# Kernel tuning notes

Hardware: AMD Instinct MI355X
Metric: run time of the kernel (lower is better)

The kernel has to match this reference:

```python
import jax, jax.numpy as jnp
import numpy as np

# 8-bit signed quantizer bounds and integer-rescale constant (from module attrs)
X1_LO, X1_HI = -128.0, 127.0
X2_LO, X2_HI = -128.0, 127.0
Y_LO, Y_HI = -128.0, 127.0
G_VALUE = 16.0


def setup_inputs() -> dict:
    key = jax.random.key(0)
    k1, k2 = jax.random.split(key)
    # Pre-quantized integer activations stored as float32 (as in int-infer mode)
    x1 = jnp.round(jnp.clip(jax.random.normal(k1, (2, 16, 2048, 64), dtype=jnp.float32) * 40.0, X1_LO, X1_HI))
    x2 = jnp.round(jnp.clip(jax.random.normal(k2, (2, 16, 64, 2048), dtype=jnp.float32) * 40.0, X2_LO, X2_HI))
    return {
        "x1": x1,
        "x2": x2,
        "scale1_last_layer": jnp.float32(0.1),
        "scale_x1": jnp.float32(0.05),
        "scale2_last_layer": jnp.float32(0.08),
        "scale_x2": jnp.float32(0.04),
    }


def _div_shift(x, scale_prev, scale_cur, lo, hi):
    # round(x * s_prev / s_cur) then clamp to quantizer bounds
    return jnp.clip(jnp.round(x * (scale_prev / scale_cur)), lo, hi)


def reference(x1, x2, scale1_last_layer, scale_x1, scale2_last_layer, scale_x2):
    # _forward_infer: rescale both operands, integer matmul, /G, round, clip
    x1_int = _div_shift(x1, scale1_last_layer, scale_x1, X1_LO, X1_HI)
    x2_int = _div_shift(x2, scale2_last_layer, scale_x2, X2_LO, X2_HI)
    # [b, h, s, d] @ [b, h, d, s] -> [b, h, s, s]
    y_int = jnp.clip(jnp.round(jnp.matmul(x1_int, x2_int) / G_VALUE), Y_LO, Y_HI)
    return y_int
```

## Files before the change

kernel.cpp:

```cpp
#include <hip/hip_runtime.h>


typedef int   v4i  __attribute__((ext_vector_type(4)));
typedef int   v16i __attribute__((ext_vector_type(16)));
typedef float v4f  __attribute__((ext_vector_type(4)));

static constexpr int BATCH = 32;
static constexpr int SEQ   = 2048;
static constexpr int DIM   = 64;
static constexpr int TILE  = 128;
static constexpr int TPB   = 256;
static constexpr int TPS   = SEQ / TILE;
static constexpr int TPBATCH = TPS * TPS;
static constexpr int NBLK  = BATCH * TPBATCH;
static constexpr size_t PKB = (size_t)BATCH * SEQ * DIM;

__device__ __forceinline__ int qpack4(v4f v, float r) {
    int dw = 0;
    #pragma unroll
    for (int j = 0; j < 4; ++j) {
        float q = rintf(v[j] * r);
        q = fminf(fmaxf(q, -128.f), 127.f);
        dw |= ((int)q & 0xFF) << (8 * j);
    }
    return dw;
}

__global__ __launch_bounds__(256) void prepack_kernel(
    const float* __restrict__ x1, const float* __restrict__ x2,
    const float* __restrict__ p_s1ll, const float* __restrict__ p_sx1,
    const float* __restrict__ p_s2ll, const float* __restrict__ p_sx2,
    char* __restrict__ A8, char* __restrict__ B8)
{
    const int bid = (int)blockIdx.x;
    const int tid = (int)threadIdx.x;
    if (bid < 1024) {
        const float r1 = p_s1ll[0] / p_sx1[0];
        const int t  = bid * 256 + tid;
        const int b  = t >> 13;
        const int m  = (t >> 2) & 2047;
        const int kq = t & 3;
        const float* src = x1 + (size_t)t * 16;
        v4i pk;
        #pragma unroll
        for (int d = 0; d < 4; ++d) pk[d] = qpack4(*(const v4f*)(src + 4 * d), r1);
        *(v4i*)(A8 + ((size_t)(b * 4 + kq) * SEQ + m) * 16) = pk;
    } else {
        const float r2 = p_s2ll[0] / p_sx2[0];
        const int t  = (bid - 1024) * 256 + tid;
        const int b  = t >> 13;
        const int kq = (t >> 11) & 3;
        const int n  = t & 2047;
        const float* src = x2 + (size_t)b * DIM * SEQ + (size_t)(kq * 16) * SEQ + n;
        v4i pk;
        #pragma unroll
        for (int d = 0; d < 4; ++d) {
            int dw = 0;
            #pragma unroll
            for (int j = 0; j < 4; ++j) {
                float q = rintf(src[(size_t)(4 * d + j) * SEQ] * r2);
                q = fminf(fmaxf(q, -128.f), 127.f);
                dw |= ((int)q & 0xFF) << (8 * j);
            }
            pk[d] = dw;
        }
        *(v4i*)(B8 + (size_t)t * 16) = pk;
    }
}

__global__ __launch_bounds__(TPB) void oint_mm_packed(
    const char* __restrict__ A8, const char* __restrict__ B8,
    float* __restrict__ out)
{
    __shared__ float slab[64 * 128];

    const int bid     = (int)blockIdx.x;
    const int logical = (bid & 7) * (NBLK >> 3) + (bid >> 3);

    const int batch = logical >> 8;
    const int t     = logical & (TPBATCH - 1);
    const int tm    = t >> 4;
    const int tn    = t & (TPS - 1);

    float* Obase = out + (size_t)batch * SEQ * SEQ;

    const int tid  = (int)threadIdx.x;
    const int lane = tid & 63;
    const int wave = tid >> 6;
    const int wr   = wave >> 1;
    const int wc   = wave & 1;

    const int mbase = tm * TILE + wr * 64;
    const int nbase = tn * TILE + wc * 64;

    const int lc = lane & 31;
    const int kh = lane >> 5;

    v4i bfrag[2][2];
    #pragma unroll
    for (int fn = 0; fn < 2; ++fn)
        #pragma unroll
        for (int s = 0; s < 2; ++s)
            bfrag[fn][s] = *(const v4i*)(
                B8 + ((size_t)(batch * 4 + s * 2 + kh) * SEQ + nbase + fn * 32 + lc) * 16);

    #pragma unroll
    for (int fm = 0; fm < 2; ++fm) {
        if (fm) __syncthreads();

        v4i af[2];
        #pragma unroll
        for (int s = 0; s < 2; ++s)
            af[s] = *(const v4i*)(
                A8 + ((size_t)(batch * 4 + s * 2 + kh) * SEQ + mbase + fm * 32 + lc) * 16);

        #pragma unroll
        for (int fn = 0; fn < 2; ++fn) {
            v16i z = {0,0,0,0,0,0,0,0,0,0,0,0,0,0,0,0};
            v16i acc = __builtin_amdgcn_mfma_i32_32x32x32_i8(af[0], bfrag[fn][0], z,   0, 0, 0);
            acc      = __builtin_amdgcn_mfma_i32_32x32x32_i8(af[1], bfrag[fn][1], acc, 0, 0, 0);

            #pragma unroll
            for (int r = 0; r < 16; ++r) {
                const int rloc = (r & 3) + 8 * (r >> 2) + 4 * kh;
                const int sr   = wr * 32 + rloc;
                const int c    = wc * 64 + fn * 32 + lc;
                float v = rintf((float)acc[r] * 0.0625f);
                v = fminf(fmaxf(v, -128.f), 127.f);
                slab[sr * 128 + c] = v;
            }
        }

        __syncthreads();

        #pragma unroll
        for (int i = 0; i < 8; ++i) {
            const int f  = i * TPB + tid;
            const int sr = f >> 5;
            const int cq = f & 31;
            v4f v = *(const v4f*)&slab[sr * 128 + cq * 4];
            const int grow = tm * TILE + ((sr >> 5) << 6) + fm * 32 + (sr & 31);
            *(v4f*)(Obase + (size_t)grow * SEQ + tn * TILE + cq * 4) = v;
        }
    }
}

extern "C" void kernel_launch(void* const* d_in, const int* in_sizes, int n_in,
                              void* d_out, int out_size, void* d_ws, size_t ws_size,
                              hipStream_t stream) {
    (void)in_sizes; (void)n_in; (void)out_size;
    const float* x1 = (const float*)d_in[0];
    const float* x2 = (const float*)d_in[1];
    const float* s1 = (const float*)d_in[2];
    const float* s2 = (const float*)d_in[3];
    const float* s3 = (const float*)d_in[4];
    const float* s4 = (const float*)d_in[5];
    float* out = (float*)d_out;

    char* A8 = (char*)d_ws;
    char* B8 = (char*)d_ws + PKB;
    prepack_kernel<<<2048, 256, 0, stream>>>(x1, x2, s1, s2, s3, s4, A8, B8);
    oint_mm_packed<<<NBLK, TPB, 0, stream>>>(A8, B8, out);
}
```

Before: 107.8 us.

## Fuse A-operand quantization into matmul kernel and use nontemporal output stores

The separate prepack of x1 into int8 is removed; the matmul kernel now reads float x1 directly and quantizes A fragments in registers before the MFMA. This drops one pass over x1 and the A8 workspace write/read, but each block re-reads and re-quantizes fp32 A rows (4x more bytes per load, repeated across 16 column tiles). Output stores become nontemporal to avoid polluting cache with the large write-once result.

```diff
diff --git a/kernel.cpp b/kernel.cpp
--- a/kernel.cpp
+++ b/kernel.cpp
@@ -26,53 +26,41 @@
     return dw;
 }
 
-__global__ __launch_bounds__(256) void prepack_kernel(
-    const float* __restrict__ x1, const float* __restrict__ x2,
-    const float* __restrict__ p_s1ll, const float* __restrict__ p_sx1,
+__global__ __launch_bounds__(256) void prepack_b_kernel(
+    const float* __restrict__ x2,
     const float* __restrict__ p_s2ll, const float* __restrict__ p_sx2,
-    char* __restrict__ A8, char* __restrict__ B8)
+    char* __restrict__ B8)
 {
-    const int bid = (int)blockIdx.x;
-    const int tid = (int)threadIdx.x;
-    if (bid < 1024) {
-        const float r1 = p_s1ll[0] / p_sx1[0];
-        const int t  = bid * 256 + tid;
-        const int b  = t >> 13;
-        const int m  = (t >> 2) & 2047;
-        const int kq = t & 3;
-        const float* src = x1 + (size_t)t * 16;
-        v4i pk;
+    const float r2 = p_s2ll[0] / p_sx2[0];
+    const int t  = (int)blockIdx.x * 256 + (int)threadIdx.x;
+    const int b  = t >> 13;
+    const int kq = (t >> 11) & 3;
+    const int n  = t & 2047;
+    const float* src = x2 + (size_t)b * DIM * SEQ + (size_t)(kq * 16) * SEQ + n;
+    v4i pk;
+    #pragma unroll
+    for (int d = 0; d < 4; ++d) {
+        int dw = 0;
         #pragma unroll
-        for (int d = 0; d < 4; ++d) pk[d] = qpack4(*(const v4f*)(src + 4 * d), r1);
-        *(v4i*)(A8 + ((size_t)(b * 4 + kq) * SEQ + m) * 16) = pk;
-    } else {
-        const float r2 = p_s2ll[0] / p_sx2[0];
-        const int t  = (bid - 1024) * 256 + tid;
-        const int b  = t >> 13;
-        const int kq = (t >> 11) & 3;
-        const int n  = t & 2047;
-        const float* src = x2 + (size_t)b * DIM * SEQ + (size_t)(kq * 16) * SEQ + n;
-        v4i pk;
-        #pragma unroll
-        for (int d = 0; d < 4; ++d) {
-            int dw = 0;
-            #pragma unroll
-            for (int j = 0; j < 4; ++j) {
-                float q = rintf(src[(size_t)(4 * d + j) * SEQ] * r2);
-                q = fminf(fmaxf(q, -128.f), 127.f);
-                dw |= ((int)q & 0xFF) << (8 * j);
-            }
-            pk[d] = dw;
+        for (int j = 0; j < 4; ++j) {
+            float q = rintf(src[(size_t)(4 * d + j) * SEQ] * r2);
+            q = fminf(fmaxf(q, -128.f), 127.f);
+            dw |= ((int)q & 0xFF) << (8 * j);
         }
-        *(v4i*)(B8 + (size_t)t * 16) = pk;
+        pk[d] = dw;
     }
+    *(v4i*)(B8 + (size_t)t * 16) = pk;
 }
 
 __global__ __launch_bounds__(TPB) void oint_mm_packed(
-    const char* __restrict__ A8, const char* __restrict__ B8,
+    const float* __restrict__ x1,
+    const float* __restrict__ p_s1ll, const float* __restrict__ p_sx1,
+    const char* __restrict__ B8,
     float* __restrict__ out)
 {
     __shared__ float slab[64 * 128];
+
+    const float r1 = p_s1ll[0] / p_sx1[0];
 
     const int bid     = (int)blockIdx.x;
     const int logical = (bid & 7) * (NBLK >> 3) + (bid >> 3);
@@ -82,7 +70,8 @@
     const int tm    = t >> 4;
     const int tn    = t & (TPS - 1);
 
-    float* Obase = out + (size_t)batch * SEQ * SEQ;
+    const float* Abase = x1 + (size_t)batch * SEQ * DIM;
+    float*       Obase = out + (size_t)batch * SEQ * SEQ;
 
     const int tid  = (int)threadIdx.x;
     const int lane = tid & 63;
@@ -110,9 +99,13 @@
 
         v4i af[2];
         #pragma unroll
-        for (int s = 0; s < 2; ++s)
-            af[s] = *(const v4i*)(
-                A8 + ((size_t)(batch * 4 + s * 2 + kh) * SEQ + mbase + fm * 32 + lc) * 16);
+        for (int s = 0; s < 2; ++s) {
+            const float* src = Abase + (size_t)(mbase + fm * 32 + lc) * DIM + s * 32 + kh * 16;
+            v4i pk;
+            #pragma unroll
+            for (int d = 0; d < 4; ++d) pk[d] = qpack4(*(const v4f*)(src + 4 * d), r1);
+            af[s] = pk;
+        }
 
         #pragma unroll
         for (int fn = 0; fn < 2; ++fn) {
@@ -140,7 +133,8 @@
             const int cq = f & 31;
             v4f v = *(const v4f*)&slab[sr * 128 + cq * 4];
             const int grow = tm * TILE + ((sr >> 5) << 6) + fm * 32 + (sr & 31);
-            *(v4f*)(Obase + (size_t)grow * SEQ + tn * TILE + cq * 4) = v;
+            __builtin_nontemporal_store(
+                v, (v4f*)(Obase + (size_t)grow * SEQ + tn * TILE + cq * 4));
         }
     }
 }
@@ -148,7 +142,7 @@
 extern "C" void kernel_launch(void* const* d_in, const int* in_sizes, int n_in,
                               void* d_out, int out_size, void* d_ws, size_t ws_size,
                               hipStream_t stream) {
-    (void)in_sizes; (void)n_in; (void)out_size;
+    (void)in_sizes; (void)n_in; (void)out_size; (void)ws_size;
     const float* x1 = (const float*)d_in[0];
     const float* x2 = (const float*)d_in[1];
     const float* s1 = (const float*)d_in[2];
@@ -157,8 +151,7 @@
     const float* s4 = (const float*)d_in[5];
     float* out = (float*)d_out;
 
-    char* A8 = (char*)d_ws;
-    char* B8 = (char*)d_ws + PKB;
-    prepack_kernel<<<2048, 256, 0, stream>>>(x1, x2, s1, s2, s3, s4, A8, B8);
-    oint_mm_packed<<<NBLK, TPB, 0, stream>>>(A8, B8, out);
+    char* B8 = (char*)d_ws;
+    prepack_b_kernel<<<1024, 256, 0, stream>>>(x2, s3, s4, B8);
+    oint_mm_packed<<<NBLK, TPB, 0, stream>>>(x1, s1, s2, B8, out);
 }
```

Result: faster. 96.18 us (-10.8%).
